# Optimization experiments

Measured on AMD Instinct MI355X. Metric: run time of the kernel, lower is better.

Reference implementation:

```python
import jax, jax.numpy as jnp
import numpy as np

EMBED_DIM = 1024
NUM_HEADS = 16
HEAD_DIM = EMBED_DIM // NUM_HEADS
B, N = 4, 2048
EPS = 1e-5


def rotate_half(x):
    x2d = x.reshape(x.shape[:-1] + (-1, 2))
    x1, x2 = x2d[..., 0], x2d[..., 1]
    return jnp.stack([-x2, x1], axis=-1).reshape(x.shape)


def apply_rotary_emb(freqs, t):
    return t * freqs[0] + rotate_half(t) * freqs[1]


def setup_inputs() -> dict:
    key = jax.random.key(0)
    ks = jax.random.split(key, 12)
    d = EMBED_DIM
    inp = {
        "x": jax.random.normal(ks[0], (B, N, d), jnp.float32),
        "encoding": jax.random.normal(ks[1], (2, N, HEAD_DIM), jnp.float32),
        "Wqkv_w": jax.random.normal(ks[2], (d, 3 * d), jnp.float32) * (1.0 / np.sqrt(d)),
        "Wqkv_b": jnp.zeros((3 * d,), jnp.float32),
        "out_w": jax.random.normal(ks[3], (d, d), jnp.float32) * (1.0 / np.sqrt(d)),
        "out_b": jnp.zeros((d,), jnp.float32),
        "ffn0_w": jax.random.normal(ks[4], (2 * d, 2 * d), jnp.float32) * (1.0 / np.sqrt(2 * d)),
        "ffn0_b": jnp.zeros((2 * d,), jnp.float32),
        "ln_scale": jnp.ones((2 * d,), jnp.float32),
        "ln_bias": jnp.zeros((2 * d,), jnp.float32),
        "ffn3_w": jax.random.normal(ks[5], (2 * d, d), jnp.float32) * (1.0 / np.sqrt(2 * d)),
        "ffn3_b": jnp.zeros((d,), jnp.float32),
    }
    return inp


def reference(x, encoding, Wqkv_w, Wqkv_b, out_w, out_b, ffn0_w, ffn0_b, ln_scale, ln_bias, ffn3_w, ffn3_b):
    b, n, d = x.shape
    # fused QKV projection
    qkv = jnp.einsum('bnd,de->bne', x, Wqkv_w) + Wqkv_b
    qkv = qkv.reshape(b, n, NUM_HEADS, HEAD_DIM, 3).transpose(0, 2, 1, 3, 4)  # (b,h,n,hd,3)
    q, k, v = qkv[..., 0], qkv[..., 1], qkv[..., 2]
    # RoPE (encoding broadcasts over batch/heads)
    q = apply_rotary_emb(encoding, q)
    k = apply_rotary_emb(encoding, k)
    # attention (no mask)
    scale = 1.0 / jnp.sqrt(jnp.asarray(HEAD_DIM, x.dtype))
    logits = jnp.einsum('bhqd,bhkd->bhqk', q, k) * scale
    attn = jax.nn.softmax(logits, axis=-1)
    context = jnp.einsum('bhqk,bhkd->bhqd', attn, v)
    message = context.transpose(0, 2, 1, 3).reshape(b, n, d)
    message = jnp.einsum('bnd,de->bne', message, out_w) + out_b
    # FFN: concat -> Dense -> LayerNorm -> GELU(exact) -> Dense
    h = jnp.concatenate([x, message], axis=-1)
    h = jnp.einsum('bnd,de->bne', h, ffn0_w) + ffn0_b
    mu = jnp.mean(h, axis=-1, keepdims=True)
    var = jnp.mean(jnp.square(h - mu), axis=-1, keepdims=True)
    h = (h - mu) * jax.lax.rsqrt(var + EPS) * ln_scale + ln_bias
    h = jax.nn.gelu(h, approximate=False)
    res = jnp.einsum('bnd,de->bne', h, ffn3_w) + ffn3_b
    return x + res
```

## Files before the change

### kernel.cpp

```cpp
#include <hip/hip_runtime.h>
#include <hip/hip_bf16.h>
#include <math.h>

typedef __bf16 bf16x8 __attribute__((ext_vector_type(8)));
typedef float f32x4 __attribute__((ext_vector_type(4)));

#define MFMA16(a, b, c) __builtin_amdgcn_mfma_f32_16x16x32_bf16((a), (b), (c), 0, 0, 0)

__device__ __forceinline__ void gload16(const void* g, void* l) {
  __builtin_amdgcn_global_load_lds((const __attribute__((address_space(1))) void*)g,
                                   (__attribute__((address_space(3))) void*)l, 16, 0, 0);
}

__global__ __launch_bounds__(256) void transpose_bf16(const float* __restrict__ in,
                                                      int ldin,
                                                      __bf16* __restrict__ out,
                                                      int ldo) {
  __shared__ float tile[32][33];
  int n0 = blockIdx.x * 32, k0 = blockIdx.y * 32;
  int tx = threadIdx.x & 31, ty = threadIdx.x >> 5;
#pragma unroll
  for (int r = 0; r < 32; r += 8)
    tile[ty + r][tx] = in[(size_t)(k0 + ty + r) * ldin + n0 + tx];
  __syncthreads();
#pragma unroll
  for (int r = 0; r < 32; r += 8)
    out[(size_t)(n0 + ty + r) * ldo + k0 + tx] = (__bf16)tile[tx][ty + r];
}

__global__ __launch_bounds__(256) void transpose_qkv_perm(const float* __restrict__ in,
                                                          __bf16* __restrict__ out) {
  __shared__ float tile[32][33];
  int n0 = blockIdx.x * 32, k0 = blockIdx.y * 32;
  int tx = threadIdx.x & 31, ty = threadIdx.x >> 5;
#pragma unroll
  for (int r = 0; r < 32; r += 8)
    tile[ty + r][tx] = in[(size_t)(k0 + ty + r) * 3072 + n0 + tx];
  __syncthreads();
#pragma unroll
  for (int r = 0; r < 32; r += 8) {
    int n = n0 + ty + r;
    int h = n / 192, rem = n % 192, hd = rem / 3, which = rem % 3;
    int np = which * 1024 + h * 64 + hd;
    out[(size_t)np * 1024 + k0 + tx] = (__bf16)tile[tx][ty + r];
  }
}

__global__ __launch_bounds__(256) void bias_perm(const float* __restrict__ b,
                                                 float* __restrict__ bp) {
  int n = blockIdx.x * 256 + threadIdx.x;
  if (n < 3072) {
    int h = n / 192, rem = n % 192, hd = rem / 3, which = rem % 3;
    bp[which * 1024 + h * 64 + hd] = b[n];
  }
}

__global__ __launch_bounds__(256) void convert_plain(const float* __restrict__ in,
                                                     __bf16* __restrict__ out) {
  int id = blockIdx.x * 256 + threadIdx.x;
  const float* src = in + (size_t)id * 8;
  __bf16 tmp[8];
#pragma unroll
  for (int e = 0; e < 8; ++e) tmp[e] = (__bf16)src[e];
  *(uint4*)(out + (size_t)id * 8) = *(uint4*)tmp;
}

__global__ __launch_bounds__(256) void convert_x(const float* __restrict__ x,
                                                 __bf16* __restrict__ h) {
  int id = blockIdx.x * 256 + threadIdx.x;
  int row = id >> 7, cc = id & 127;
  const float* src = x + (size_t)row * 1024 + cc * 8;
  __bf16 tmp[8];
#pragma unroll
  for (int e = 0; e < 8; ++e) tmp[e] = (__bf16)src[e];
  *(uint4*)(h + (size_t)row * 2048 + cc * 8) = *(uint4*)tmp;
}

__global__ __launch_bounds__(256) void fuse_bias_part(const float* __restrict__ bout,
                                                      const float* __restrict__ w0,
                                                      float* __restrict__ part) {
  int n = blockIdx.x * 256 + threadIdx.x;
  int e0 = blockIdx.y * 64;
  float s = 0.f;
#pragma unroll 4
  for (int e = 0; e < 64; ++e)
    s += bout[e0 + e] * w0[(size_t)(1024 + e0 + e) * 2048 + n];
  part[(size_t)blockIdx.y * 2048 + n] = s;
}

__global__ __launch_bounds__(256) void fuse_bias_red(const float* __restrict__ part,
                                                     const float* __restrict__ b0,
                                                     float* __restrict__ bf) {
  int n = blockIdx.x * 256 + threadIdx.x;
  float s = b0[n];
#pragma unroll
  for (int y = 0; y < 16; ++y) s += part[(size_t)y * 2048 + n];
  bf[n] = s;
}

template <typename OutT, bool HAS_RES, bool HAS_BIAS>
__global__ __launch_bounds__(256) void gemm_kernel(
    const __bf16* __restrict__ A, int lda,
    const __bf16* __restrict__ Bt,
    const float* __restrict__ bias,
    OutT* __restrict__ C, int ldc,
    const float* __restrict__ res,
    int M, int Nn, int K) {
  __shared__ __attribute__((aligned(16))) __bf16 As[128 * 64];
  __shared__ __attribute__((aligned(16))) __bf16 Bs[128 * 64];

  const int t = threadIdx.x;
  const int row0A = blockIdx.x * 128;
  const int row0B = blockIdx.y * 128;
  const int wave = t >> 6, lane = t & 63;
  const int wm = wave >> 1, wn = wave & 1;
  const int g = lane >> 4, lr = lane & 15;

  f32x4 acc[4][4] = {};

  for (int k0 = 0; k0 < K; k0 += 64) {
#pragma unroll
    for (int p = 0; p < 4; ++p) {
      int cbase = (wave * 4 + p) * 64;
      int ci = cbase + lane;
      int r = ci >> 3, cp = ci & 7, cl = cp ^ (r & 7);
      gload16(A + (size_t)(row0A + r) * lda + k0 + cl * 8, &As[cbase * 8]);
      gload16(Bt + (size_t)(row0B + r) * K + k0 + cl * 8, &Bs[cbase * 8]);
    }
    __syncthreads();
#pragma unroll
    for (int kk = 0; kk < 2; ++kk) {
      bf16x8 af[4], bfr[4];
#pragma unroll
      for (int mt = 0; mt < 4; ++mt) {
        int r = wm * 64 + mt * 16 + lr, c = kk * 4 + g;
        af[mt] = *(const bf16x8*)((char*)As + r * 128 + ((c ^ (r & 7)) * 16));
      }
#pragma unroll
      for (int nt = 0; nt < 4; ++nt) {
        int r = wn * 64 + nt * 16 + lr, c = kk * 4 + g;
        bfr[nt] = *(const bf16x8*)((char*)Bs + r * 128 + ((c ^ (r & 7)) * 16));
      }
#pragma unroll
      for (int mt = 0; mt < 4; ++mt)
#pragma unroll
        for (int nt = 0; nt < 4; ++nt)
          acc[mt][nt] = MFMA16(af[mt], bfr[nt], acc[mt][nt]);
    }
    __syncthreads();
  }

  float bias_v[4];
#pragma unroll
  for (int nt = 0; nt < 4; ++nt)
    bias_v[nt] = HAS_BIAS ? bias[row0B + wn * 64 + nt * 16 + lr] : 0.f;
#pragma unroll
  for (int mt = 0; mt < 4; ++mt) {
    int grow_base = row0A + wm * 64 + mt * 16 + g * 4;
#pragma unroll
    for (int nt = 0; nt < 4; ++nt) {
      int gcol = row0B + wn * 64 + nt * 16 + lr;
#pragma unroll
      for (int j = 0; j < 4; ++j) {
        int grow = grow_base + j;
        float v = acc[mt][nt][j] + bias_v[nt];
        if (HAS_RES) v += res[(size_t)grow * ldc + gcol];
        C[(size_t)grow * ldc + gcol] = (OutT)v;
      }
    }
  }
}

__global__ __launch_bounds__(256) void rope_scatter(
    const __bf16* __restrict__ qkv, const float* __restrict__ enc,
    __bf16* __restrict__ q, __bf16* __restrict__ kk, __bf16* __restrict__ vt) {
  int bh = blockIdx.y;
  int b = bh >> 4, h = bh & 15;
  int n0 = blockIdx.x * 64;
  int t = threadIdx.x;
  const float QSC = 0.125f * 1.44269504088896f;
#pragma unroll
  for (int i = 0; i < 2; ++i) {
    int id = t + i * 256;
    int nl = id >> 3, cc = id & 7;
    int n = n0 + nl;
    size_t row = (size_t)(b * 2048 + n) * 3072;
    bf16x8 qv = *(const bf16x8*)(qkv + row + h * 64 + cc * 8);
    bf16x8 kv = *(const bf16x8*)(qkv + row + 1024 + h * 64 + cc * 8);
    const float* e0 = enc + (size_t)n * 64 + cc * 8;
    const float* e1 = e0 + 131072;
    __bf16 qo[8], ko[8];
#pragma unroll
    for (int e = 0; e < 8; e += 2) {
      float q0 = (float)qv[e], q1 = (float)qv[e + 1];
      float k0 = (float)kv[e], k1 = (float)kv[e + 1];
      float f00 = e0[e], f01 = e0[e + 1], f10 = e1[e], f11 = e1[e + 1];
      qo[e] = (__bf16)((q0 * f00 - q1 * f10) * QSC);
      qo[e + 1] = (__bf16)((q1 * f01 + q0 * f11) * QSC);
      ko[e] = (__bf16)(k0 * f00 - k1 * f10);
      ko[e + 1] = (__bf16)(k1 * f01 + k0 * f11);
    }
    size_t qb = ((size_t)bh * 2048 + n) * 64 + cc * 8;
    *(uint4*)(q + qb) = *(uint4*)qo;
    *(uint4*)(kk + qb) = *(uint4*)ko;
  }
#pragma unroll
  for (int i = 0; i < 2; ++i) {
    int id = t + i * 256;
    int hd = id >> 3, c = id & 7;
    __bf16 tmp[8];
#pragma unroll
    for (int e = 0; e < 8; ++e) {
      int kv = (c >> 2) * 32 + (e >> 2) * 16 + (c & 3) * 4 + (e & 3);
      int n = n0 + kv;
      tmp[e] = qkv[(size_t)(b * 2048 + n) * 3072 + 2048 + h * 64 + hd];
    }
    *(uint4*)(vt + ((size_t)bh * 64 + hd) * 2048 + n0 + c * 8) = *(uint4*)tmp;
  }
}

__global__ __launch_bounds__(256) void attn_kernel(
    const __bf16* __restrict__ q, const __bf16* __restrict__ k,
    const __bf16* __restrict__ vt, __bf16* __restrict__ ctx) {
  __shared__ __attribute__((aligned(16))) __bf16 Ks[2][64 * 64];
  __shared__ __attribute__((aligned(16))) __bf16 Vs[2][64 * 64];

  int nwg = gridDim.x * gridDim.y;
  int bid0 = blockIdx.y * gridDim.x + blockIdx.x;
  int bid = (bid0 & 7) * (nwg >> 3) + (bid0 >> 3);
  const int bh = bid / gridDim.x, qblk = bid % gridDim.x;
  const int b = bh >> 4, h = bh & 15;
  const int q0 = qblk * 64;
  const int t = threadIdx.x, wave = t >> 6, lane = t & 63;
  const int g = lane >> 4, lr = lane & 15;
  const int qrow = q0 + wave * 16;

  const __bf16* kbase = k + (size_t)bh * 2048 * 64;
  const __bf16* vbase = vt + (size_t)bh * 64 * 2048;

  bf16x8 qf[2];
#pragma unroll
  for (int kc = 0; kc < 2; ++kc)
    qf[kc] = *(const bf16x8*)(q + ((size_t)bh * 2048 + qrow + lr) * 64 + kc * 32 + g * 8);

  bf16x8 ones;
#pragma unroll
  for (int e = 0; e < 8; ++e) ones[e] = (__bf16)1.0f;

  f32x4 o[4] = {};
  f32x4 lacc = {};

#define STAGE_ATTN(buf, kv0)                                                    \
  {                                                                             \
    _Pragma("unroll") for (int p = 0; p < 2; ++p) {                             \
      int cbase = wave * 128 + p * 64;                                          \
      int ci = cbase + lane;                                                    \
      int r = ci >> 3, cp = ci & 7, cl = cp ^ (r & 7);                          \
      gload16(kbase + (size_t)((kv0) + r) * 64 + cl * 8, &Ks[buf][cbase * 8]);  \
      gload16(vbase + (size_t)r * 2048 + (kv0) + cl * 8, &Vs[buf][cbase * 8]);  \
    }                                                                           \
  }

  STAGE_ATTN(0, 0);
  __syncthreads();
  int buf = 0;

  for (int kv0 = 0; kv0 < 2048; kv0 += 64) {
    if (kv0 + 64 < 2048) STAGE_ATTN(buf ^ 1, kv0 + 64);

    f32x4 s[4];
    __builtin_amdgcn_s_setprio(1);
#pragma unroll
    for (int nt = 0; nt < 4; ++nt) {
      int r = nt * 16 + lr;
      bf16x8 kf0 = *(const bf16x8*)((char*)Ks[buf] + r * 128 + ((g ^ (r & 7)) * 16));
      bf16x8 kf1 = *(const bf16x8*)((char*)Ks[buf] + r * 128 + (((4 + g) ^ (r & 7)) * 16));
      f32x4 a = {};
      a = MFMA16(kf0, qf[0], a);
      a = MFMA16(kf1, qf[1], a);
      s[nt] = a;
    }
    __builtin_amdgcn_s_setprio(0);

#pragma unroll
    for (int t2 = 0; t2 < 2; ++t2) {
      bf16x8 pf;
#pragma unroll
      for (int e = 0; e < 8; ++e)
        pf[e] = (__bf16)__builtin_amdgcn_exp2f(s[2 * t2 + (e >> 2)][e & 3]);
      lacc = MFMA16(ones, pf, lacc);
      __builtin_amdgcn_s_setprio(1);
#pragma unroll
      for (int nt = 0; nt < 4; ++nt) {
        int r = nt * 16 + lr;
        bf16x8 vf = *(const bf16x8*)((char*)Vs[buf] + r * 128 + (((t2 * 4 + g) ^ (r & 7)) * 16));
        o[nt] = MFMA16(vf, pf, o[nt]);
      }
      __builtin_amdgcn_s_setprio(0);
    }
    __syncthreads();
    buf ^= 1;
  }

  float inv = 1.f / lacc[0];

  size_t obase = ((size_t)(b * 2048 + qrow + lr)) * 2048 + 1024 + h * 64;
#pragma unroll
  for (int nt = 0; nt < 4; ++nt) {
    __bf16 w4[4];
#pragma unroll
    for (int j = 0; j < 4; ++j) w4[j] = (__bf16)(o[nt][j] * inv);
    *(uint2*)(ctx + obase + nt * 16 + g * 4) = *(uint2*)w4;
  }
#undef STAGE_ATTN
}

__global__ __launch_bounds__(256) void ln_gelu(const __bf16* __restrict__ hin,
                                               const float* __restrict__ lns,
                                               const float* __restrict__ lnb,
                                               __bf16* __restrict__ hout) {
  int row = blockIdx.x;
  const __bf16* rp = hin + (size_t)row * 2048;
  int t = threadIdx.x;
  __bf16 tmp[8];
  *(uint4*)tmp = *(const uint4*)(rp + t * 8);
  float vals[8], s = 0.f, s2 = 0.f;
#pragma unroll
  for (int e = 0; e < 8; ++e) {
    float x = (float)tmp[e];
    vals[e] = x;
    s += x;
    s2 += x * x;
  }
#pragma unroll
  for (int m = 1; m < 64; m <<= 1) {
    s += __shfl_xor(s, m, 64);
    s2 += __shfl_xor(s2, m, 64);
  }
  __shared__ float red[8];
  int wave = t >> 6, lane = t & 63;
  if (lane == 0) { red[wave] = s; red[4 + wave] = s2; }
  __syncthreads();
  s = red[0] + red[1] + red[2] + red[3];
  s2 = red[4] + red[5] + red[6] + red[7];
  float mu = s * (1.f / 2048.f);
  float var = s2 * (1.f / 2048.f) - mu * mu;
  float rstd = rsqrtf(var + 1e-5f);
  __bf16 outv[8];
#pragma unroll
  for (int e = 0; e < 8; ++e) {
    int c = t * 8 + e;
    float xh = (vals[e] - mu) * rstd * lns[c] + lnb[c];
    float gg = 0.5f * xh * (1.f + erff(xh * 0.70710678118f));
    outv[e] = (__bf16)gg;
  }
  *(uint4*)(hout + (size_t)row * 2048 + t * 8) = *(uint4*)outv;
}

extern "C" void kernel_launch(void* const* d_in, const int* in_sizes, int n_in,
                              void* d_out, int out_size, void* d_ws, size_t ws_size,
                              hipStream_t stream) {
  const float* x = (const float*)d_in[0];
  const float* enc = (const float*)d_in[1];
  const float* wqkv = (const float*)d_in[2];
  const float* bqkv = (const float*)d_in[3];
  const float* wout = (const float*)d_in[4];
  const float* bout = (const float*)d_in[5];
  const float* wffn0 = (const float*)d_in[6];
  const float* bffn0 = (const float*)d_in[7];
  const float* lns = (const float*)d_in[8];
  const float* lnb = (const float*)d_in[9];
  const float* wffn3 = (const float*)d_in[10];
  const float* bffn3 = (const float*)d_in[11];
  float* out = (float*)d_out;
  char* ws = (char*)d_ws;

  __bf16* wT_qkv = (__bf16*)(ws + 0);
  __bf16* wT_ffn0 = (__bf16*)(ws + 6291456);
  __bf16* wT_ffn3 = (__bf16*)(ws + 14680064);
  __bf16* wout_bf = (__bf16*)(ws + 18874368);
  __bf16* w0bT = (__bf16*)(ws + 20971520);
  float* bias_part = (float*)(ws + 20971520);
  float* bqkv_p = (float*)(ws + 25165824);
  float* bffn0_f = (float*)(ws + 25178112);
  __bf16* h_in = (__bf16*)(ws + 25186304);
  __bf16* qkv = (__bf16*)(ws + 58740736);
  __bf16* ffn0o = qkv;
  __bf16* qb = (__bf16*)(ws + 109072384);
  __bf16* h2 = qb;
  __bf16* kb = (__bf16*)(ws + 125849600);
  __bf16* vtb = (__bf16*)(ws + 142626816);

  dim3 blk(256);
  transpose_qkv_perm<<<dim3(96, 32), blk, 0, stream>>>(wqkv, wT_qkv);
  bias_perm<<<12, blk, 0, stream>>>(bqkv, bqkv_p);
  transpose_bf16<<<dim3(64, 32), blk, 0, stream>>>(wffn0, 2048, wT_ffn0, 2048);
  transpose_bf16<<<dim3(64, 32), blk, 0, stream>>>(wffn0 + (size_t)1024 * 2048, 2048,
                                                   w0bT, 1024);
  transpose_bf16<<<dim3(32, 64), blk, 0, stream>>>(wffn3, 1024, wT_ffn3, 2048);
  convert_plain<<<512, blk, 0, stream>>>(wout, wout_bf);
  gemm_kernel<__bf16, false, false><<<dim3(16, 8), blk, 0, stream>>>(
      w0bT, 1024, wout_bf, nullptr, wT_ffn0 + 1024, 2048, nullptr, 2048, 1024, 1024);
  fuse_bias_part<<<dim3(8, 16), blk, 0, stream>>>(bout, wffn0, bias_part);
  fuse_bias_red<<<8, blk, 0, stream>>>(bias_part, bffn0, bffn0_f);
  convert_x<<<4096, blk, 0, stream>>>(x, h_in);

  gemm_kernel<__bf16, false, true><<<dim3(64, 24), blk, 0, stream>>>(
      h_in, 2048, wT_qkv, bqkv_p, qkv, 3072, nullptr, 8192, 3072, 1024);

  rope_scatter<<<dim3(32, 64), blk, 0, stream>>>(qkv, enc, qb, kb, vtb);
  attn_kernel<<<dim3(32, 64), blk, 0, stream>>>(qb, kb, vtb, h_in);

  gemm_kernel<__bf16, false, true><<<dim3(64, 16), blk, 0, stream>>>(
      h_in, 2048, wT_ffn0, bffn0_f, ffn0o, 2048, nullptr, 8192, 2048, 2048);

  ln_gelu<<<8192, blk, 0, stream>>>(ffn0o, lns, lnb, h2);

  gemm_kernel<float, true, true><<<dim3(64, 8), blk, 0, stream>>>(
      h2, 2048, wT_ffn3, bffn3, out, 1024, x, 8192, 1024, 2048);
}
```

Before: 417.2 us.

## Add 256x256-tile 8-wave pipelined GEMM for QKV and FFN0 projections

Adds a new GEMM kernel with 256x256 output tiles, 512 threads and double-buffered LDS filled by direct global-to-LDS loads. The K-loop is split into four MFMA quadrants, with next-tile loads interleaved between them and MFMA priority raised during compute. The QKV and first FFN projections now use it in place of the 128-tile kernel, aiming for more reuse per byte loaded and better overlap of loads with MFMA. The cost is higher register and LDS pressure and fewer blocks, which can hurt wave balance across the CUs.

```diff
diff --git a/kernel.cpp b/kernel.cpp
--- a/kernel.cpp
+++ b/kernel.cpp
@@ -11,6 +11,8 @@
   __builtin_amdgcn_global_load_lds((const __attribute__((address_space(1))) void*)g,
                                    (__attribute__((address_space(3))) void*)l, 16, 0, 0);
 }
+
+#define BARRIER asm volatile("s_barrier" ::: "memory")
 
 __global__ __launch_bounds__(256) void transpose_bf16(const float* __restrict__ in,
                                                       int ldin,
@@ -167,6 +169,157 @@
         if (HAS_RES) v += res[(size_t)grow * ldc + gcol];
         C[(size_t)grow * ldc + gcol] = (OutT)v;
       }
+    }
+  }
+}
+
+template <typename OutT>
+__global__ __launch_bounds__(512, 2) void gemm256p(
+    const __bf16* __restrict__ A, int lda,
+    const __bf16* __restrict__ Bt, int ldb,
+    const float* __restrict__ bias,
+    OutT* __restrict__ C, int ldc, int K) {
+  __shared__ __attribute__((aligned(16))) __bf16 As[2][256 * 64];
+  __shared__ __attribute__((aligned(16))) __bf16 Bs[2][256 * 64];
+
+  const int t = threadIdx.x;
+  const int wave = t >> 6, lane = t & 63;
+  const int wm = wave >> 2, wn = wave & 3;
+  const int g = lane >> 4, lr = lane & 15;
+  const int row0A = blockIdx.x * 256, row0B = blockIdx.y * 256;
+  const int L = K >> 6;
+
+  f32x4 acc[8][4] = {};
+
+#define STG_A(tile, i)                                                        \
+  {                                                                           \
+    int cb = ((i) * 8 + wave) * 64;                                           \
+    int ci = cb + lane;                                                       \
+    int r = ci >> 3, cl = (ci & 7) ^ (r & 7);                                 \
+    gload16(A + (size_t)(row0A + r) * lda + (size_t)(tile) * 64 + cl * 8,     \
+            &As[(tile) & 1][cb * 8]);                                         \
+  }
+#define STG_B(tile, i)                                                        \
+  {                                                                           \
+    int cb = ((i) * 8 + wave) * 64;                                           \
+    int ci = cb + lane;                                                       \
+    int r = ci >> 3, cl = (ci & 7) ^ (r & 7);                                 \
+    gload16(Bt + (size_t)(row0B + r) * ldb + (size_t)(tile) * 64 + cl * 8,    \
+            &Bs[(tile) & 1][cb * 8]);                                         \
+  }
+#define AFRAG(d, mi, ks)                                                      \
+  (*(const bf16x8*)((const char*)As[d] + (wm * 128 + (mi) * 16 + lr) * 128 +  \
+                    ((((ks) * 4 + g) ^ (lr & 7)) * 16)))
+#define BFRAG(d, ni, ks)                                                      \
+  (*(const bf16x8*)((const char*)Bs[d] + (wn * 64 + (ni) * 16 + lr) * 128 +   \
+                    ((((ks) * 4 + g) ^ (lr & 7)) * 16)))
+
+#pragma unroll
+  for (int i = 0; i < 4; ++i) STG_A(0, i);
+#pragma unroll
+  for (int i = 0; i < 4; ++i) STG_B(0, i);
+  STG_A(1, 0);
+  STG_A(1, 1);
+  asm volatile("s_waitcnt vmcnt(2)" ::: "memory");
+  BARRIER;
+
+  for (int tt = 0; tt < L; ++tt) {
+    const int d = tt & 1;
+    const bool s1 = (tt + 1) < L, s2 = (tt + 2) < L;
+    bf16x8 aL[4][2], aH[4][2], bL[2][2], bH[2][2];
+
+#pragma unroll
+    for (int mi = 0; mi < 4; ++mi) {
+      aL[mi][0] = AFRAG(d, mi, 0);
+      aL[mi][1] = AFRAG(d, mi, 1);
+    }
+#pragma unroll
+    for (int ni = 0; ni < 2; ++ni) {
+      bL[ni][0] = BFRAG(d, ni, 0);
+      bL[ni][1] = BFRAG(d, ni, 1);
+    }
+    if (s1) { STG_A(tt + 1, 2); STG_A(tt + 1, 3); }
+    BARRIER;
+    __builtin_amdgcn_s_setprio(1);
+#pragma unroll
+    for (int mi = 0; mi < 4; ++mi)
+#pragma unroll
+      for (int ni = 0; ni < 2; ++ni) {
+        acc[mi][ni] = MFMA16(aL[mi][0], bL[ni][0], acc[mi][ni]);
+        acc[mi][ni] = MFMA16(aL[mi][1], bL[ni][1], acc[mi][ni]);
+      }
+    __builtin_amdgcn_s_setprio(0);
+    BARRIER;
+
+#pragma unroll
+    for (int ni = 0; ni < 2; ++ni) {
+      bH[ni][0] = BFRAG(d, ni + 2, 0);
+      bH[ni][1] = BFRAG(d, ni + 2, 1);
+    }
+    if (s1) { STG_B(tt + 1, 0); STG_B(tt + 1, 1); }
+    BARRIER;
+    __builtin_amdgcn_s_setprio(1);
+#pragma unroll
+    for (int mi = 0; mi < 4; ++mi)
+#pragma unroll
+      for (int ni = 0; ni < 2; ++ni) {
+        acc[mi][ni + 2] = MFMA16(aL[mi][0], bH[ni][0], acc[mi][ni + 2]);
+        acc[mi][ni + 2] = MFMA16(aL[mi][1], bH[ni][1], acc[mi][ni + 2]);
+      }
+    __builtin_amdgcn_s_setprio(0);
+    BARRIER;
+
+#pragma unroll
+    for (int mi = 0; mi < 4; ++mi) {
+      aH[mi][0] = AFRAG(d, mi + 4, 0);
+      aH[mi][1] = AFRAG(d, mi + 4, 1);
+    }
+    if (s1) { STG_B(tt + 1, 2); STG_B(tt + 1, 3); }
+    BARRIER;
+    __builtin_amdgcn_s_setprio(1);
+#pragma unroll
+    for (int mi = 0; mi < 4; ++mi)
+#pragma unroll
+      for (int ni = 0; ni < 2; ++ni) {
+        acc[mi + 4][ni + 2] = MFMA16(aH[mi][0], bH[ni][0], acc[mi + 4][ni + 2]);
+        acc[mi + 4][ni + 2] = MFMA16(aH[mi][1], bH[ni][1], acc[mi + 4][ni + 2]);
+      }
+    __builtin_amdgcn_s_setprio(0);
+    BARRIER;
+
+    if (s2) { STG_A(tt + 2, 0); STG_A(tt + 2, 1); }
+    __builtin_amdgcn_s_setprio(1);
+#pragma unroll
+    for (int mi = 0; mi < 4; ++mi)
+#pragma unroll
+      for (int ni = 0; ni < 2; ++ni) {
+        acc[mi + 4][ni] = MFMA16(aH[mi][0], bL[ni][0], acc[mi + 4][ni]);
+        acc[mi + 4][ni] = MFMA16(aH[mi][1], bL[ni][1], acc[mi + 4][ni]);
+      }
+    __builtin_amdgcn_s_setprio(0);
+    if (s2)
+      asm volatile("s_waitcnt vmcnt(2)" ::: "memory");
+    else
+      asm volatile("s_waitcnt vmcnt(0)" ::: "memory");
+    BARRIER;
+  }
+#undef STG_A
+#undef STG_B
+#undef AFRAG
+#undef BFRAG
+
+  float bias_v[4];
+#pragma unroll
+  for (int ni = 0; ni < 4; ++ni) bias_v[ni] = bias[row0B + wn * 64 + ni * 16 + lr];
+#pragma unroll
+  for (int mi = 0; mi < 8; ++mi) {
+    int grow_base = row0A + wm * 128 + mi * 16 + g * 4;
+#pragma unroll
+    for (int ni = 0; ni < 4; ++ni) {
+      int gcol = row0B + wn * 64 + ni * 16 + lr;
+#pragma unroll
+      for (int j = 0; j < 4; ++j)
+        C[(size_t)(grow_base + j) * ldc + gcol] = (OutT)(acc[mi][ni][j] + bias_v[ni]);
     }
   }
 }
@@ -405,14 +558,14 @@
   fuse_bias_red<<<8, blk, 0, stream>>>(bias_part, bffn0, bffn0_f);
   convert_x<<<4096, blk, 0, stream>>>(x, h_in);
 
-  gemm_kernel<__bf16, false, true><<<dim3(64, 24), blk, 0, stream>>>(
-      h_in, 2048, wT_qkv, bqkv_p, qkv, 3072, nullptr, 8192, 3072, 1024);
+  gemm256p<__bf16><<<dim3(32, 12), dim3(512), 0, stream>>>(
+      h_in, 2048, wT_qkv, 1024, bqkv_p, qkv, 3072, 1024);
 
   rope_scatter<<<dim3(32, 64), blk, 0, stream>>>(qkv, enc, qb, kb, vtb);
   attn_kernel<<<dim3(32, 64), blk, 0, stream>>>(qb, kb, vtb, h_in);
 
-  gemm_kernel<__bf16, false, true><<<dim3(64, 16), blk, 0, stream>>>(
-      h_in, 2048, wT_ffn0, bffn0_f, ffn0o, 2048, nullptr, 8192, 2048, 2048);
+  gemm256p<__bf16><<<dim3(32, 8), dim3(512), 0, stream>>>(
+      h_in, 2048, wT_ffn0, 2048, bffn0_f, ffn0o, 2048, 2048);
 
   ln_gelu<<<8192, blk, 0, stream>>>(ffn0o, lns, lnb, h2);
 
```

Measured after the change: 405.1 us. 2.9% less time.
